# Kernel tuning notes

Measured on AMD Instinct MI355X. Metric: run time of the kernel, lower is better.

## Reference

```python
import jax, jax.numpy as jnp
import numpy as np

B, T, F = 2048, 96, 32
H = 1024
G_EMB = 16
LSTM_IN = F + 11 + 1 + G_EMB  # 60


def _lstm_cell(x, h, c, W_ih, W_hh, b):
    g = x @ W_ih.T + h @ W_hh.T + b
    i, f, gg, o = jnp.split(g, 4, axis=-1)  # torch gate order: i, f, g, o
    c_new = jax.nn.sigmoid(f) * c + jax.nn.sigmoid(i) * jnp.tanh(gg)
    h_new = jax.nn.sigmoid(o) * jnp.tanh(c_new)
    return h_new, c_new


def setup_inputs() -> dict:
    key = jax.random.key(0)
    ks = jax.random.split(key, 26)
    s = 1.0 / np.sqrt(H)
    inp = {
        "dec_known": jax.random.normal(ks[0], (B, T, F), jnp.float32),
        "target_y": jax.random.normal(ks[1], (B, T, 1), jnp.float32),
        "enc_h": jax.random.normal(ks[2], (2, B, H), jnp.float32),
        "enc_c": jax.random.normal(ks[3], (2, B, H), jnp.float32),
        "last_enc_consumption": jax.random.normal(ks[4], (B, 1), jnp.float32),
        "group_ids": jax.random.randint(ks[5], (B,), 0, 1000),
        "cat_province": jax.random.randint(ks[6], (B,), 0, 13),
        "cat_customer_type": jax.random.randint(ks[7], (B,), 0, 2),
        "cat_price_type": jax.random.randint(ks[8], (B,), 0, 5),
        "cat_consumption_level": jax.random.randint(ks[9], (B,), 0, 3),
        # learned parameters
        "group_emb": jax.random.normal(ks[10], (1000, G_EMB), jnp.float32),
        "emb_province": jax.random.normal(ks[11], (13, 4), jnp.float32),
        "emb_customer_type": jax.random.normal(ks[12], (2, 2), jnp.float32),
        "emb_price_type": jax.random.normal(ks[13], (5, 3), jnp.float32),
        "emb_consumption_level": jax.random.normal(ks[14], (3, 2), jnp.float32),
        "W_ih0": jax.random.normal(ks[15], (4 * H, LSTM_IN), jnp.float32) * s,
        "W_hh0": jax.random.normal(ks[16], (4 * H, H), jnp.float32) * s,
        "b0": jax.random.normal(ks[17], (4 * H,), jnp.float32) * s,
        "W_ih1": jax.random.normal(ks[18], (4 * H, H), jnp.float32) * s,
        "W_hh1": jax.random.normal(ks[19], (4 * H, H), jnp.float32) * s,
        "b1": jax.random.normal(ks[20], (4 * H,), jnp.float32) * s,
        "W_proj": jax.random.normal(ks[21], (1, H), jnp.float32) * s,
        "b_proj": jnp.zeros((1,), jnp.float32),
    }
    return inp


def reference(dec_known, target_y, enc_h, enc_c, last_enc_consumption,
              group_ids, cat_province, cat_customer_type, cat_price_type,
              cat_consumption_level, group_emb, emb_province, emb_customer_type,
              emb_price_type, emb_consumption_level, W_ih0, W_hh0, b0,
              W_ih1, W_hh1, b1, W_proj, b_proj):
    b, t, _ = dec_known.shape
    # static per-sample features (categorical + group embeddings)
    cat_emb = jnp.concatenate([
        emb_province[cat_province], emb_customer_type[cat_customer_type],
        emb_price_type[cat_price_type], emb_consumption_level[cat_consumption_level],
    ], axis=-1)  # [B, 11]
    group_vec = group_emb[group_ids]  # [B, 16]
    static = jnp.concatenate([cat_emb, group_vec], axis=-1)  # [B, 27]
    # teacher_forcing_ratio = 1.0 => prev_y is last_enc_consumption then target_y shifted
    prev_y = jnp.concatenate([last_enc_consumption[:, None, :], target_y[:, :-1, :]], axis=1)  # [B,T,1]
    x = jnp.concatenate([
        prev_y, dec_known,
        jnp.broadcast_to(static[:, None, :], (b, t, static.shape[-1])),
    ], axis=-1)  # [B, T, 60]

    def step(carry, x_t):
        h1, c1, h2, c2 = carry
        h1, c1 = _lstm_cell(x_t, h1, c1, W_ih0, W_hh0, b0)
        h2, c2 = _lstm_cell(h1, h2, c2, W_ih1, W_hh1, b1)
        return (h1, c1, h2, c2), h2

    init = (enc_h[0], enc_c[0], enc_h[1], enc_c[1])
    _, hs = jax.lax.scan(step, init, jnp.swapaxes(x, 0, 1))  # hs: [T, B, H]
    y = jnp.einsum('tbh,oh->bto', hs, W_proj) + b_proj  # [B, T, 1]
    return y
```

## Files before the change

kernel.cpp:

```cpp
#include <hip/hip_runtime.h>
#include <hip/hip_bf16.h>
#include <stdint.h>


#define BB  2048
#define TT  96
#define NG  4096
#define KL1 1088
#define KL2 2048

typedef __bf16 bf16;
typedef __bf16 bf16x8 __attribute__((ext_vector_type(8)));
typedef float  f32x4  __attribute__((ext_vector_type(4)));

__device__ __forceinline__ float sigm(float x) { return 1.0f / (1.0f + __expf(-x)); }
__device__ __forceinline__ float ftanh(float x) { return 2.0f / (1.0f + __expf(-2.0f * x)) - 1.0f; }

__device__ __forceinline__ void gload16(const bf16* g, bf16* l) {
  __builtin_amdgcn_global_load_lds((const __attribute__((address_space(1))) void*)g,
                                   (__attribute__((address_space(3))) void*)l, 16, 0, 0);
}

#define SB() __builtin_amdgcn_sched_barrier(0)


__global__ __launch_bounds__(256) void build_w0(const float* __restrict__ Wih0,
                                                const float* __restrict__ Whh0,
                                                bf16* __restrict__ W0) {
  int idx = blockIdx.x * 256 + threadIdx.x;
  if (idx >= NG * KL1) return;
  int np = idx / KL1, k = idx % KL1;
  int n = (np & 3) * 1024 + (np >> 2);
  float v;
  if (k < 60)       v = Wih0[n * 60 + k];
  else if (k < 64)  v = 0.0f;
  else              v = Whh0[n * 1024 + (k - 64)];
  W0[idx] = (bf16)v;
}

__global__ __launch_bounds__(256) void build_w1(const float* __restrict__ Wih1,
                                                const float* __restrict__ Whh1,
                                                bf16* __restrict__ W1) {
  int idx = blockIdx.x * 256 + threadIdx.x;
  if (idx >= NG * KL2) return;
  int np = idx >> 11, k = idx & 2047;
  int n = (np & 3) * 1024 + (np >> 2);
  float v = (k < 1024) ? Wih1[n * 1024 + k] : Whh1[n * 1024 + (k - 1024)];
  W1[idx] = (bf16)v;
}

__global__ __launch_bounds__(256) void perm_bias(const float* __restrict__ b0,
                                                 const float* __restrict__ b1,
                                                 float* __restrict__ b0p,
                                                 float* __restrict__ b1p) {
  int idx = blockIdx.x * 256 + threadIdx.x;
  if (idx >= NG) return;
  int n = (idx & 3) * 1024 + (idx >> 2);
  b0p[idx] = b0[n];
  b1p[idx] = b1[n];
}

__global__ __launch_bounds__(256) void build_x(
    const float* __restrict__ dec, const float* __restrict__ ty, const float* __restrict__ lec,
    const int* __restrict__ gid, const int* __restrict__ cp, const int* __restrict__ cct,
    const int* __restrict__ cpt, const int* __restrict__ ccl,
    const float* __restrict__ gemb, const float* __restrict__ ep, const float* __restrict__ ect,
    const float* __restrict__ ept, const float* __restrict__ ecl,
    bf16* __restrict__ X) {
  int idx = blockIdx.x * 256 + threadIdx.x;
  if (idx >= BB * TT) return;
  int b = idx / TT, t = idx % TT;
  bf16* x = X + (size_t)idx * 64;
  x[0] = (bf16)((t == 0) ? lec[b] : ty[b * TT + t - 1]);
  const float* d = dec + (size_t)idx * 32;
  #pragma unroll
  for (int k = 0; k < 32; ++k) x[1 + k] = (bf16)d[k];
  const float* e;
  e = ep  + cp[b]  * 4;  for (int j = 0; j < 4;  ++j) x[33 + j] = (bf16)e[j];
  e = ect + cct[b] * 2;  for (int j = 0; j < 2;  ++j) x[37 + j] = (bf16)e[j];
  e = ept + cpt[b] * 3;  for (int j = 0; j < 3;  ++j) x[39 + j] = (bf16)e[j];
  e = ecl + ccl[b] * 2;  for (int j = 0; j < 2;  ++j) x[42 + j] = (bf16)e[j];
  e = gemb + gid[b] * 16; for (int j = 0; j < 16; ++j) x[44 + j] = (bf16)e[j];
  for (int j = 60; j < 64; ++j) x[j] = (bf16)0.0f;
}

__global__ __launch_bounds__(256) void init_state(const float* __restrict__ enc_h,
                                                  const float* __restrict__ enc_c,
                                                  bf16* __restrict__ H1b,
                                                  bf16* __restrict__ H2b,
                                                  float* __restrict__ c1t,
                                                  float* __restrict__ c2t) {
  int idx = blockIdx.x * 256 + threadIdx.x;
  if (idx >= BB * 1024) return;
  int b = idx >> 10, h = idx & 1023;
  H1b[idx] = (bf16)enc_h[idx];
  H2b[idx] = (bf16)enc_h[(size_t)BB * 1024 + idx];
  c1t[(size_t)h * BB + b] = enc_c[idx];
  c2t[(size_t)h * BB + b] = enc_c[(size_t)BB * 1024 + idx];
}


template <int MODE>
__device__ __forceinline__ void gemm_cell_body(
    int tm, int tn, int t,
    const bf16* __restrict__ P0, const bf16* __restrict__ P1,
    const bf16* __restrict__ Wt, const float* __restrict__ bperm,
    float* __restrict__ ct, bf16* __restrict__ Hout,
    const float* __restrict__ wp, const float* __restrict__ bp,
    float* __restrict__ y,
    bf16* As, bf16* Ws) {
  constexpr int KT = (MODE == 0) ? KL1 : KL2;
  constexpr int NT = KT / 32;

  int tid = threadIdx.x;
  int lane = tid & 63;
  int w = tid >> 6;
  int wb = (w & 3) << 6;
  int wg = (w >> 2) << 6;

  f32x4 acc[4][4];
  #pragma unroll
  for (int mw = 0; mw < 4; ++mw)
    #pragma unroll
    for (int nb = 0; nb < 4; ++nb) acc[mw][nb] = (f32x4){0.f, 0.f, 0.f, 0.f};

  int rA0 = tid >> 2, rA1 = (512 + tid) >> 2, rW = tid >> 2;
  int kcA0 = (((tid & 3) ^ ((rA0 >> 1) & 3)) << 3);
  int kcA1 = (((tid & 3) ^ ((rA1 >> 1) & 3)) << 3);
  int kcW  = kcA0;
  int dA0 = (tid & ~63) * 8;
  int dA1 = 4096 + dA0;
  int dW  = dA0;

  auto aptr = [&](int row, int gk) -> const bf16* {
    if constexpr (MODE == 0) {
      return (gk < 64) ? (P0 + ((size_t)(tm + row) * TT + t) * 64 + gk)
                       : (P1 + (size_t)(tm + row) * 1024 + (gk - 64));
    } else {
      return (gk < 1024) ? (P0 + (size_t)(tm + row) * 1024 + gk)
                         : (P1 + (size_t)(tm + row) * 1024 + (gk - 1024));
    }
  };
  auto stage = [&](int kt, int buf) {
    int gk0 = kt * 32 + kcA0, gk1 = kt * 32 + kcA1, gkw = kt * 32 + kcW;
    gload16(aptr(rA0, gk0), As + buf * 8192 + dA0);
    gload16(aptr(rA1, gk1), As + buf * 8192 + dA1);
    gload16(Wt + (size_t)(tn + rW) * KT + gkw, Ws + buf * 4096 + dW);
  };

  stage(0, 0);
  __syncthreads();

  int lrow = lane & 15;
  int klocal = ((((lane >> 4) ^ (lrow >> 1)) & 3) << 3);

  for (int kt = 0; kt < NT; ++kt) {
    int buf = kt & 1;
    if (kt + 1 < NT) stage(kt + 1, buf ^ 1);
    SB();

    bf16x8 af[4], wf[4];
    #pragma unroll
    for (int nb = 0; nb < 4; ++nb)
      af[nb] = *reinterpret_cast<const bf16x8*>(&As[buf * 8192 + (wb + nb * 16 + lrow) * 32 + klocal]);
    #pragma unroll
    for (int mw = 0; mw < 4; ++mw)
      wf[mw] = *reinterpret_cast<const bf16x8*>(&Ws[buf * 4096 + (wg + mw * 16 + lrow) * 32 + klocal]);

    __builtin_amdgcn_s_setprio(1);
    #pragma unroll
    for (int mw = 0; mw < 4; ++mw)
      #pragma unroll
      for (int nb = 0; nb < 4; ++nb)
        acc[mw][nb] = __builtin_amdgcn_mfma_f32_16x16x32_bf16(wf[mw], af[nb], acc[mw][nb], 0, 0, 0);
    __builtin_amdgcn_s_setprio(0);

    __syncthreads();
  }

  bf16* hst = As + w * 1024;
  int u = lane >> 4;
  int bl = lane & 15;
  int hwave = (tn + wg) >> 2;
  int bgb = tm + wb;
  float yp[4] = {0.f, 0.f, 0.f, 0.f};

  #pragma unroll
  for (int mw = 0; mw < 4; ++mw) {
    int hg = hwave + mw * 4 + u;
    f32x4 bv = *reinterpret_cast<const f32x4*>(&bperm[hg * 4]);
    float wph = 0.f;
    if constexpr (MODE == 1) wph = wp[hg];
    #pragma unroll
    for (int nb = 0; nb < 4; ++nb) {
      int bg = bgb + nb * 16 + bl;
      float gi = acc[mw][nb][0] + bv[0];
      float gf = acc[mw][nb][1] + bv[1];
      float gg = acc[mw][nb][2] + bv[2];
      float go = acc[mw][nb][3] + bv[3];
      float* cp_ = ct + (size_t)hg * BB + bg;
      float c = *cp_;
      float cn = sigm(gf) * c + sigm(gi) * ftanh(gg);
      float hn = sigm(go) * ftanh(cn);
      *cp_ = cn;
      hst[(nb * 16 + bl) * 16 + mw * 4 + u] = (bf16)hn;
      if constexpr (MODE == 1) yp[nb] += hn * wph;
    }
  }

  asm volatile("s_waitcnt lgkmcnt(0)" ::: "memory");
  SB();

  #pragma unroll
  for (int q = 0; q < 2; ++q) {
    int chunk = q * 64 + lane;
    int row = chunk >> 1, half = chunk & 1;
    bf16x8 v = *reinterpret_cast<const bf16x8*>(&hst[row * 16 + half * 8]);
    *reinterpret_cast<bf16x8*>(&Hout[(size_t)(bgb + row) * 1024 + hwave + half * 8]) = v;
  }

  if constexpr (MODE == 1) {
    #pragma unroll
    for (int nb = 0; nb < 4; ++nb) {
      float s = yp[nb];
      s += __shfl_xor(s, 16);
      s += __shfl_xor(s, 32);
      if (lane < 16)
        atomicAdd(&y[(size_t)(bgb + nb * 16 + lane) * TT + t], s);
    }
  } else {
    if (tn == 0 && tid < 256) y[(size_t)(tm + tid) * TT + t] = bp[0];
  }
}

__global__ __launch_bounds__(512, 4) void step_kernel(
    const bf16* __restrict__ H1in, const bf16* __restrict__ H2in,
    bf16* __restrict__ H1out, bf16* __restrict__ H2out,
    const bf16* __restrict__ X,
    const bf16* __restrict__ W0, const bf16* __restrict__ W1,
    const float* __restrict__ b0p, const float* __restrict__ b1p,
    float* __restrict__ c1t, float* __restrict__ c2t,
    const float* __restrict__ wp, const float* __restrict__ bp,
    float* __restrict__ y, int t2, int only_l1) {
  __shared__ alignas(16) bf16 As[2 * 8192];
  __shared__ alignas(16) bf16 Ws[2 * 4096];
  int bid = (int)blockIdx.x;
  int v = bid & 255;
  int x = v & 7, j = v >> 3;
  int tm = (j & 7) << 8;
  int tn = ((x << 2) + (j >> 3)) << 7;
  if (only_l1 || bid >= 256) {
    int t1 = t2 + 1;
    if (t1 >= TT) return;
    gemm_cell_body<0>(tm, tn, t1, X, H1in, W0, b0p, c1t, H1out, nullptr, bp, y, As, Ws);
  } else {
    gemm_cell_body<1>(tm, tn, t2, H1in, H2in, W1, b1p, c2t, H2out, wp, nullptr, y, As, Ws);
  }
}


extern "C" void kernel_launch(void* const* d_in, const int* in_sizes, int n_in,
                              void* d_out, int out_size, void* d_ws, size_t ws_size,
                              hipStream_t stream) {
  const float* dec   = (const float*)d_in[0];
  const float* ty    = (const float*)d_in[1];
  const float* enc_h = (const float*)d_in[2];
  const float* enc_c = (const float*)d_in[3];
  const float* lec   = (const float*)d_in[4];
  const int*   gid   = (const int*)d_in[5];
  const int*   cp    = (const int*)d_in[6];
  const int*   cct   = (const int*)d_in[7];
  const int*   cpt   = (const int*)d_in[8];
  const int*   ccl   = (const int*)d_in[9];
  const float* gemb  = (const float*)d_in[10];
  const float* ep    = (const float*)d_in[11];
  const float* ect   = (const float*)d_in[12];
  const float* ept   = (const float*)d_in[13];
  const float* ecl   = (const float*)d_in[14];
  const float* Wih0  = (const float*)d_in[15];
  const float* Whh0  = (const float*)d_in[16];
  const float* b0    = (const float*)d_in[17];
  const float* Wih1  = (const float*)d_in[18];
  const float* Whh1  = (const float*)d_in[19];
  const float* b1    = (const float*)d_in[20];
  const float* wp    = (const float*)d_in[21];
  const float* bp    = (const float*)d_in[22];
  float* y = (float*)d_out;

  char* ws = (char*)d_ws;
  bf16* W0    = (bf16*)ws;  ws += (size_t)NG * KL1 * 2;
  bf16* W1    = (bf16*)ws;  ws += (size_t)NG * KL2 * 2;
  bf16* X     = (bf16*)ws;  ws += (size_t)BB * TT * 64 * 2;
  bf16* H1a   = (bf16*)ws;  ws += (size_t)BB * 1024 * 2;
  bf16* H1b   = (bf16*)ws;  ws += (size_t)BB * 1024 * 2;
  bf16* H2a   = (bf16*)ws;  ws += (size_t)BB * 1024 * 2;
  bf16* H2b   = (bf16*)ws;  ws += (size_t)BB * 1024 * 2;
  float* c1t  = (float*)ws; ws += (size_t)BB * 1024 * 4;
  float* c2t  = (float*)ws; ws += (size_t)BB * 1024 * 4;
  float* b0p  = (float*)ws; ws += (size_t)NG * 4;
  float* b1p  = (float*)ws; ws += (size_t)NG * 4;

  build_w0<<<(NG * KL1 + 255) / 256, 256, 0, stream>>>(Wih0, Whh0, W0);
  build_w1<<<(NG * KL2 + 255) / 256, 256, 0, stream>>>(Wih1, Whh1, W1);
  perm_bias<<<NG / 256, 256, 0, stream>>>(b0, b1, b0p, b1p);
  build_x<<<(BB * TT + 255) / 256, 256, 0, stream>>>(dec, ty, lec, gid, cp, cct, cpt, ccl,
                                                     gemb, ep, ect, ept, ecl, X);
  init_state<<<(BB * 1024) / 256, 256, 0, stream>>>(enc_h, enc_c, H1b, H2b, c1t, c2t);

  step_kernel<<<256, 512, 0, stream>>>(H1b, nullptr, H1a, nullptr, X, W0, W1,
                                       b0p, b1p, c1t, c2t, wp, bp, y, -1, 1);
  for (int t = 0; t < TT; ++t) {
    bf16* h1i = (t & 1) ? H1b : H1a;
    bf16* h1o = (t & 1) ? H1a : H1b;
    bf16* h2i = (t & 1) ? H2a : H2b;
    bf16* h2o = (t & 1) ? H2b : H2a;
    step_kernel<<<512, 512, 0, stream>>>(h1i, h2i, h1o, h2o, X, W0, W1,
                                         b0p, b1p, c1t, c2t, wp, bp, y, t, 0);
  }
}
```

Measured before the change: 6.880 ms.

## Pre-swizzle weights into MFMA fragment order and load them directly to registers

Weights are repacked once into a per-panel, per-k-tile layout that matches the MFMA operand fragments, so each wave reads its weight fragments straight from global memory into registers instead of staging them through LDS. The block shrinks from 512 to 256 threads with a 128x128 tile. Layer-2 uses 512 blocks and layer-1 uses 256 blocks that each handle two N tiles back to back, for 768 blocks per step. The K loop becomes a two-deep pipeline: activations go through LDS via global_load_lds, weights are double-buffered in registers, and explicit vmcnt waits and raw barriers control ordering. This cuts LDS traffic and footprint but relies on L2 to serve repeated weight reads, and the hand-written waitcnt accounting is fragile.

```diff
diff --git a/kernel.cpp b/kernel.cpp
--- a/kernel.cpp
+++ b/kernel.cpp
@@ -6,8 +6,8 @@
 #define BB  2048
 #define TT  96
 #define NG  4096
-#define KL1 1088
-#define KL2 2048
+#define NT0 34
+#define NT1 64
 
 typedef __bf16 bf16;
 typedef __bf16 bf16x8 __attribute__((ext_vector_type(8)));
@@ -21,32 +21,41 @@
                                    (__attribute__((address_space(3))) void*)l, 16, 0, 0);
 }
 
-#define SB() __builtin_amdgcn_sched_barrier(0)
-
-
-__global__ __launch_bounds__(256) void build_w0(const float* __restrict__ Wih0,
-                                                const float* __restrict__ Whh0,
-                                                bf16* __restrict__ W0) {
-  int idx = blockIdx.x * 256 + threadIdx.x;
-  if (idx >= NG * KL1) return;
-  int np = idx / KL1, k = idx % KL1;
-  int n = (np & 3) * 1024 + (np >> 2);
+#define SB()  __builtin_amdgcn_sched_barrier(0)
+#define BAR() __builtin_amdgcn_s_barrier()
+
+
+__global__ __launch_bounds__(256) void build_wf1(const float* __restrict__ Wih1,
+                                                 const float* __restrict__ Whh1,
+                                                 bf16* __restrict__ Wf) {
+  int idx = blockIdx.x * 256 + threadIdx.x;
+  if (idx >= 32 * NT1 * 4096) return;
+  int j = idx & 7, lane = (idx >> 3) & 63, mw = (idx >> 9) & 3;
+  int wg = (idx >> 11) & 1, kt = (idx >> 12) & 63, panel = idx >> 18;
+  int np = panel * 128 + wg * 64 + mw * 16 + (lane & 15);
+  int k  = kt * 32 + ((lane >> 4) << 3) + j;
+  int n  = (np & 3) * 1024 + (np >> 2);
+  float v = (k < 1024) ? Wih1[n * 1024 + k] : Whh1[n * 1024 + (k - 1024)];
+  Wf[idx] = (bf16)v;
+}
+
+__global__ __launch_bounds__(256) void build_wf0(const float* __restrict__ Wih0,
+                                                 const float* __restrict__ Whh0,
+                                                 bf16* __restrict__ Wf) {
+  int idx = blockIdx.x * 256 + threadIdx.x;
+  if (idx >= 32 * NT0 * 4096) return;
+  int j = idx & 7, lane = (idx >> 3) & 63, mw = (idx >> 9) & 3;
+  int wg = (idx >> 11) & 1;
+  int rem = idx >> 12;
+  int kt = rem % NT0, panel = rem / NT0;
+  int np = panel * 128 + wg * 64 + mw * 16 + (lane & 15);
+  int k  = kt * 32 + ((lane >> 4) << 3) + j;
+  int n  = (np & 3) * 1024 + (np >> 2);
   float v;
-  if (k < 60)       v = Wih0[n * 60 + k];
-  else if (k < 64)  v = 0.0f;
-  else              v = Whh0[n * 1024 + (k - 64)];
-  W0[idx] = (bf16)v;
-}
-
-__global__ __launch_bounds__(256) void build_w1(const float* __restrict__ Wih1,
-                                                const float* __restrict__ Whh1,
-                                                bf16* __restrict__ W1) {
-  int idx = blockIdx.x * 256 + threadIdx.x;
-  if (idx >= NG * KL2) return;
-  int np = idx >> 11, k = idx & 2047;
-  int n = (np & 3) * 1024 + (np >> 2);
-  float v = (k < 1024) ? Wih1[n * 1024 + k] : Whh1[n * 1024 + (k - 1024)];
-  W1[idx] = (bf16)v;
+  if (k < 60)      v = Wih0[n * 60 + k];
+  else if (k < 64) v = 0.0f;
+  else             v = Whh0[n * 1024 + (k - 64)];
+  Wf[idx] = (bf16)v;
 }
 
 __global__ __launch_bounds__(256) void perm_bias(const float* __restrict__ b0,
@@ -101,22 +110,20 @@
 
 
 template <int MODE>
-__device__ __forceinline__ void gemm_cell_body(
+__device__ __forceinline__ void body(
     int tm, int tn, int t,
     const bf16* __restrict__ P0, const bf16* __restrict__ P1,
-    const bf16* __restrict__ Wt, const float* __restrict__ bperm,
+    const bf16* __restrict__ Wf, const float* __restrict__ bperm,
     float* __restrict__ ct, bf16* __restrict__ Hout,
     const float* __restrict__ wp, const float* __restrict__ bp,
-    float* __restrict__ y,
-    bf16* As, bf16* Ws) {
-  constexpr int KT = (MODE == 0) ? KL1 : KL2;
-  constexpr int NT = KT / 32;
-
-  int tid = threadIdx.x;
-  int lane = tid & 63;
-  int w = tid >> 6;
-  int wb = (w & 3) << 6;
-  int wg = (w >> 2) << 6;
+    float* __restrict__ y, bf16* As)
+{
+  constexpr int NT = MODE ? NT1 : NT0;
+
+  const int tid = threadIdx.x;
+  const int lane = tid & 63, w = tid >> 6;
+  const int lrow = lane & 15, u = lane >> 4;
+  const int wb = w & 1, wg = w >> 1;
 
   f32x4 acc[4][4];
   #pragma unroll
@@ -124,76 +131,86 @@
     #pragma unroll
     for (int nb = 0; nb < 4; ++nb) acc[mw][nb] = (f32x4){0.f, 0.f, 0.f, 0.f};
 
-  int rA0 = tid >> 2, rA1 = (512 + tid) >> 2, rW = tid >> 2;
-  int kcA0 = (((tid & 3) ^ ((rA0 >> 1) & 3)) << 3);
-  int kcA1 = (((tid & 3) ^ ((rA1 >> 1) & 3)) << 3);
-  int kcW  = kcA0;
-  int dA0 = (tid & ~63) * 8;
-  int dA1 = 4096 + dA0;
-  int dW  = dA0;
-
-  auto aptr = [&](int row, int gk) -> const bf16* {
+  const int r0 = tid >> 2, r1 = (256 + tid) >> 2;
+  const int kc0 = (((tid & 3) ^ ((r0 >> 1) & 3)) << 3);
+  const int kc1 = (((tid & 3) ^ ((r1 >> 1) & 3)) << 3);
+  const int d0 = (tid & ~63) * 8;
+  const int d1 = 2048 + d0;
+  const int klocal = ((((lane >> 4) ^ (lrow >> 1)) & 3) << 3);
+
+  auto aptr = [&](int row, int kt, int kc) -> const bf16* {
     if constexpr (MODE == 0) {
-      return (gk < 64) ? (P0 + ((size_t)(tm + row) * TT + t) * 64 + gk)
-                       : (P1 + (size_t)(tm + row) * 1024 + (gk - 64));
+      return (kt < 2) ? (P0 + ((size_t)(tm + row) * TT + t) * 64 + kt * 32 + kc)
+                      : (P1 + (size_t)(tm + row) * 1024 + (kt - 2) * 32 + kc);
     } else {
-      return (gk < 1024) ? (P0 + (size_t)(tm + row) * 1024 + gk)
-                         : (P1 + (size_t)(tm + row) * 1024 + (gk - 1024));
+      return (kt < 32) ? (P0 + (size_t)(tm + row) * 1024 + kt * 32 + kc)
+                       : (P1 + (size_t)(tm + row) * 1024 + (kt - 32) * 32 + kc);
     }
   };
-  auto stage = [&](int kt, int buf) {
-    int gk0 = kt * 32 + kcA0, gk1 = kt * 32 + kcA1, gkw = kt * 32 + kcW;
-    gload16(aptr(rA0, gk0), As + buf * 8192 + dA0);
-    gload16(aptr(rA1, gk1), As + buf * 8192 + dA1);
-    gload16(Wt + (size_t)(tn + rW) * KT + gkw, Ws + buf * 4096 + dW);
+  auto stageA = [&](int kt, bf16* buf) {
+    gload16(aptr(r0, kt, kc0), buf + d0);
+    gload16(aptr(r1, kt, kc1), buf + d1);
   };
 
-  stage(0, 0);
-  __syncthreads();
-
-  int lrow = lane & 15;
-  int klocal = ((((lane >> 4) ^ (lrow >> 1)) & 3) << 3);
-
-  for (int kt = 0; kt < NT; ++kt) {
-    int buf = kt & 1;
-    if (kt + 1 < NT) stage(kt + 1, buf ^ 1);
+  const bf16* wfbase = Wf + ((size_t)(tn >> 7) * NT) * 4096 + wg * 2048 + lane * 8;
+  auto loadW = [&](bf16x8 (&wf)[4], int kt) {
+    const bf16* p = wfbase + (size_t)kt * 4096;
+    #pragma unroll
+    for (int mw = 0; mw < 4; ++mw)
+      wf[mw] = *reinterpret_cast<const bf16x8*>(p + mw * 512);
+  };
+
+  bf16x8 wfA[4], wfB[4];
+
+  stageA(0, As);
+  loadW(wfA, 0);
+  stageA(1, As + 4096);
+  asm volatile("s_waitcnt vmcnt(2)" ::: "memory");
+  SB(); BAR(); SB();
+
+  auto iter = [&](int kt, bf16x8 (&cur)[4], bf16x8 (&nxt)[4]) {
+    bf16* buf = As + ((kt & 1) ? 4096 : 0);
+    bf16x8 af[4];
+    #pragma unroll
+    for (int nb = 0; nb < 4; ++nb)
+      af[nb] = *reinterpret_cast<const bf16x8*>(&buf[(wb * 64 + nb * 16 + lrow) * 32 + klocal]);
+    asm volatile("s_waitcnt lgkmcnt(0)" ::: "memory");
+    SB(); BAR(); SB();
+    if (kt + 2 < NT) stageA(kt + 2, buf);
+    if (kt + 1 < NT) loadW(nxt, kt + 1);
     SB();
-
-    bf16x8 af[4], wf[4];
-    #pragma unroll
-    for (int nb = 0; nb < 4; ++nb)
-      af[nb] = *reinterpret_cast<const bf16x8*>(&As[buf * 8192 + (wb + nb * 16 + lrow) * 32 + klocal]);
-    #pragma unroll
-    for (int mw = 0; mw < 4; ++mw)
-      wf[mw] = *reinterpret_cast<const bf16x8*>(&Ws[buf * 4096 + (wg + mw * 16 + lrow) * 32 + klocal]);
-
     __builtin_amdgcn_s_setprio(1);
     #pragma unroll
     for (int mw = 0; mw < 4; ++mw)
       #pragma unroll
       for (int nb = 0; nb < 4; ++nb)
-        acc[mw][nb] = __builtin_amdgcn_mfma_f32_16x16x32_bf16(wf[mw], af[nb], acc[mw][nb], 0, 0, 0);
+        acc[mw][nb] = __builtin_amdgcn_mfma_f32_16x16x32_bf16(cur[mw], af[nb], acc[mw][nb], 0, 0, 0);
     __builtin_amdgcn_s_setprio(0);
-
-    __syncthreads();
+    if (kt + 2 < NT)      { asm volatile("s_waitcnt vmcnt(6)" ::: "memory"); }
+    else if (kt + 1 < NT) { asm volatile("s_waitcnt vmcnt(4)" ::: "memory"); }
+    else                  { asm volatile("s_waitcnt vmcnt(0)" ::: "memory"); }
+    SB(); BAR(); SB();
+  };
+
+  for (int kt = 0; kt < NT; kt += 2) {
+    iter(kt,     wfA, wfB);
+    iter(kt + 1, wfB, wfA);
   }
 
   bf16* hst = As + w * 1024;
-  int u = lane >> 4;
-  int bl = lane & 15;
-  int hwave = (tn + wg) >> 2;
-  int bgb = tm + wb;
+  const int hq = (tn >> 2) + wg * 16;
+  const int bgb = tm + wb * 64;
   float yp[4] = {0.f, 0.f, 0.f, 0.f};
 
   #pragma unroll
   for (int mw = 0; mw < 4; ++mw) {
-    int hg = hwave + mw * 4 + u;
+    int hg = hq + mw * 4 + u;
     f32x4 bv = *reinterpret_cast<const f32x4*>(&bperm[hg * 4]);
     float wph = 0.f;
     if constexpr (MODE == 1) wph = wp[hg];
     #pragma unroll
     for (int nb = 0; nb < 4; ++nb) {
-      int bg = bgb + nb * 16 + bl;
+      int bg = bgb + nb * 16 + lrow;
       float gi = acc[mw][nb][0] + bv[0];
       float gf = acc[mw][nb][1] + bv[1];
       float gg = acc[mw][nb][2] + bv[2];
@@ -203,7 +220,7 @@
       float cn = sigm(gf) * c + sigm(gi) * ftanh(gg);
       float hn = sigm(go) * ftanh(cn);
       *cp_ = cn;
-      hst[(nb * 16 + bl) * 16 + mw * 4 + u] = (bf16)hn;
+      hst[(nb * 16 + lrow) * 16 + mw * 4 + u] = (bf16)hn;
       if constexpr (MODE == 1) yp[nb] += hn * wph;
     }
   }
@@ -216,7 +233,7 @@
     int chunk = q * 64 + lane;
     int row = chunk >> 1, half = chunk & 1;
     bf16x8 v = *reinterpret_cast<const bf16x8*>(&hst[row * 16 + half * 8]);
-    *reinterpret_cast<bf16x8*>(&Hout[(size_t)(bgb + row) * 1024 + hwave + half * 8]) = v;
+    *reinterpret_cast<bf16x8*>(&Hout[(size_t)(bgb + row) * 1024 + hq + half * 8]) = v;
   }
 
   if constexpr (MODE == 1) {
@@ -229,32 +246,36 @@
         atomicAdd(&y[(size_t)(bgb + nb * 16 + lane) * TT + t], s);
     }
   } else {
-    if (tn == 0 && tid < 256) y[(size_t)(tm + tid) * TT + t] = bp[0];
-  }
-}
-
-__global__ __launch_bounds__(512, 4) void step_kernel(
+    if (tn == 0 && tid < 128) y[(size_t)(tm + tid) * TT + t] = bp[0];
+  }
+}
+
+__global__ __launch_bounds__(256, 3) void step_kernel(
     const bf16* __restrict__ H1in, const bf16* __restrict__ H2in,
     bf16* __restrict__ H1out, bf16* __restrict__ H2out,
     const bf16* __restrict__ X,
-    const bf16* __restrict__ W0, const bf16* __restrict__ W1,
+    const bf16* __restrict__ Wf0, const bf16* __restrict__ Wf1,
     const float* __restrict__ b0p, const float* __restrict__ b1p,
     float* __restrict__ c1t, float* __restrict__ c2t,
     const float* __restrict__ wp, const float* __restrict__ bp,
     float* __restrict__ y, int t2, int only_l1) {
-  __shared__ alignas(16) bf16 As[2 * 8192];
-  __shared__ alignas(16) bf16 Ws[2 * 4096];
+  __shared__ alignas(16) bf16 As[2 * 4096];
   int bid = (int)blockIdx.x;
-  int v = bid & 255;
-  int x = v & 7, j = v >> 3;
-  int tm = (j & 7) << 8;
-  int tn = ((x << 2) + (j >> 3)) << 7;
-  if (only_l1 || bid >= 256) {
+  if (only_l1 || bid >= 512) {
+    int v = only_l1 ? bid : bid - 512;
     int t1 = t2 + 1;
     if (t1 >= TT) return;
-    gemm_cell_body<0>(tm, tn, t1, X, H1in, W0, b0p, c1t, H1out, nullptr, bp, y, As, Ws);
+    int x = v & 7, j = v >> 3;
+    int tm  = (j & 15) << 7;
+    int tn0 = ((x << 1) + (j >> 4)) << 8;
+    body<0>(tm, tn0, t1, X, H1in, Wf0, b0p, c1t, H1out, nullptr, bp, y, As);
+    __syncthreads();
+    body<0>(tm, tn0 + 128, t1, X, H1in, Wf0, b0p, c1t, H1out, nullptr, bp, y, As);
   } else {
-    gemm_cell_body<1>(tm, tn, t2, H1in, H2in, W1, b1p, c2t, H2out, wp, nullptr, y, As, Ws);
+    int x = bid & 7, j = bid >> 3;
+    int tm = (j & 15) << 7;
+    int tn = ((x << 2) + (j >> 4)) << 7;
+    body<1>(tm, tn, t2, H1in, H2in, Wf1, b1p, c2t, H2out, wp, nullptr, y, As);
   }
 }
 
@@ -288,8 +309,8 @@
   float* y = (float*)d_out;
 
   char* ws = (char*)d_ws;
-  bf16* W0    = (bf16*)ws;  ws += (size_t)NG * KL1 * 2;
-  bf16* W1    = (bf16*)ws;  ws += (size_t)NG * KL2 * 2;
+  bf16* Wf1   = (bf16*)ws;  ws += (size_t)32 * NT1 * 4096 * 2;
+  bf16* Wf0   = (bf16*)ws;  ws += (size_t)32 * NT0 * 4096 * 2;
   bf16* X     = (bf16*)ws;  ws += (size_t)BB * TT * 64 * 2;
   bf16* H1a   = (bf16*)ws;  ws += (size_t)BB * 1024 * 2;
   bf16* H1b   = (bf16*)ws;  ws += (size_t)BB * 1024 * 2;
@@ -300,21 +321,21 @@
   float* b0p  = (float*)ws; ws += (size_t)NG * 4;
   float* b1p  = (float*)ws; ws += (size_t)NG * 4;
 
-  build_w0<<<(NG * KL1 + 255) / 256, 256, 0, stream>>>(Wih0, Whh0, W0);
-  build_w1<<<(NG * KL2 + 255) / 256, 256, 0, stream>>>(Wih1, Whh1, W1);
+  build_wf1<<<(32 * NT1 * 4096) / 256, 256, 0, stream>>>(Wih1, Whh1, Wf1);
+  build_wf0<<<(32 * NT0 * 4096 + 255) / 256, 256, 0, stream>>>(Wih0, Whh0, Wf0);
   perm_bias<<<NG / 256, 256, 0, stream>>>(b0, b1, b0p, b1p);
   build_x<<<(BB * TT + 255) / 256, 256, 0, stream>>>(dec, ty, lec, gid, cp, cct, cpt, ccl,
                                                      gemb, ep, ect, ept, ecl, X);
   init_state<<<(BB * 1024) / 256, 256, 0, stream>>>(enc_h, enc_c, H1b, H2b, c1t, c2t);
 
-  step_kernel<<<256, 512, 0, stream>>>(H1b, nullptr, H1a, nullptr, X, W0, W1,
+  step_kernel<<<256, 256, 0, stream>>>(H1b, nullptr, H1a, nullptr, X, Wf0, Wf1,
                                        b0p, b1p, c1t, c2t, wp, bp, y, -1, 1);
   for (int t = 0; t < TT; ++t) {
     bf16* h1i = (t & 1) ? H1b : H1a;
     bf16* h1o = (t & 1) ? H1a : H1b;
     bf16* h2i = (t & 1) ? H2a : H2b;
     bf16* h2o = (t & 1) ? H2b : H2a;
-    step_kernel<<<512, 512, 0, stream>>>(h1i, h2i, h1o, h2o, X, W0, W1,
+    step_kernel<<<768, 256, 0, stream>>>(h1i, h2i, h1o, h2o, X, Wf0, Wf1,
                                          b0p, b1p, c1t, c2t, wp, bp, y, t, 0);
   }
 }
```

Measured after the change: 6.973 ms. Within noise of the previous version (+1.4%).
